# Performance work log

Hardware: AMD Instinct MI355X
Metric: run time of the kernel (lower is better)

## Reference

```python
import jax, jax.numpy as jnp
import numpy as np

TOKENS, DIM, N_EXPERTS, TOPK = 8192, 4096, 256, 8

def setup_inputs() -> dict:
    key = jax.random.key(0)
    k1, k2 = jax.random.split(key)
    x = jax.random.normal(k1, (TOKENS, DIM), dtype=jnp.float32)
    weight = jax.random.normal(k2, (N_EXPERTS, DIM), dtype=jnp.float32) * (DIM ** -0.5)
    return {"x": x, "weight": weight}

def reference(x, weight):
    # logits: [tokens, n_experts]
    logits = jnp.einsum('td,ed->te', x, weight)
    scores = jax.nn.sigmoid(logits)
    topv, indices = jax.lax.top_k(scores, TOPK)          # [tokens, topk]
    gates = topv / jnp.sum(topv, axis=-1, keepdims=True)
    return gates, indices
```

## Files before the change

kernel.cpp:

```cpp
#include <hip/hip_runtime.h>
#include <hip/hip_bf16.h>
#include <hip/hip_fp16.h>
#include <math.h>

#define TOKENS   8192
#define DIM      4096
#define NEXP     256
#define TOPK     8
#define CAND     12

#define MT4      128
#define BK3      64
#define KG       (DIM / 32)

typedef _Float16 f16x8 __attribute__((ext_vector_type(8)));
typedef float    f32x4 __attribute__((ext_vector_type(4)));

typedef const __attribute__((address_space(1))) unsigned int* gas_ptr;
typedef       __attribute__((address_space(3))) unsigned int* las_ptr;

__global__ __launch_bounds__(256)
void convert_w(const float* __restrict__ w, _Float16* __restrict__ whs) {
    const int g = blockIdx.x * 256 + threadIdx.x;
    const int tile = g >> 6, c = g & 63;
    const int q = c >> 4, r = c & 15;
    const int ng = tile / KG, kg = tile % KG;
    const int n = ng * 16 + r, k = kg * 32 + q * 8;
    const float4 a = *(const float4*)(w + (size_t)n * DIM + k);
    const float4 b = *(const float4*)(w + (size_t)n * DIM + k + 4);
    f16x8 h;
    h[0] = (_Float16)a.x; h[1] = (_Float16)a.y;
    h[2] = (_Float16)a.z; h[3] = (_Float16)a.w;
    h[4] = (_Float16)b.x; h[5] = (_Float16)b.y;
    h[6] = (_Float16)b.z; h[7] = (_Float16)b.w;
    *(f16x8*)(whs + (size_t)g * 8) = h;
}

__global__ __launch_bounds__(512, 1)
void gemm_v4(const float* __restrict__ x, const _Float16* __restrict__ whs,
             float* __restrict__ logits, int kspan) {
    __shared__ _Float16 As[2][16 * 512];
    __shared__ _Float16 Bs[2][32 * 512];

    const int t = threadIdx.x, w = t >> 6, lane = t & 63;
    const int wm = w >> 2, wn = w & 3;
    const int m0 = blockIdx.x * MT4;
    const int kb = blockIdx.y * kspan;
    const int kend = kb + kspan;
    float* lp    = logits + (size_t)blockIdx.y * TOKENS * NEXP;

    const int am  = t >> 2;
    const int ack = (t & 3) * 2;
    const int amg = am >> 4, amr = am & 15;
    const int aoff0 = ((amg * 2 + (ack >> 2)) * 64 + (ack & 3) * 16 + amr) * 8;
    const int ack1  = ack + 1;
    const int aoff1 = ((amg * 2 + (ack1 >> 2)) * 64 + (ack1 & 3) * 16 + amr) * 8;

    f32x4 acc[4][4];
    #pragma unroll
    for (int i = 0; i < 4; ++i)
        #pragma unroll
        for (int j = 0; j < 4; ++j) acc[i][j] = (f32x4){0.f, 0.f, 0.f, 0.f};

    const float* xrow = x + (size_t)(m0 + am) * DIM + ack * 8;

    auto stage_B = [&](int buf, int k0) {
        #pragma unroll
        for (int c = 0; c < 4; ++c) {
            const int ti  = w * 4 + c;
            const int ng  = ti >> 1, kgl = ti & 1;
            const _Float16* gp = whs + ((size_t)(ng * KG + (k0 >> 5) + kgl)) * 512
                                     + lane * 8;
            __builtin_amdgcn_global_load_lds((gas_ptr)gp,
                                             (las_ptr)&Bs[buf][ti * 512],
                                             16, 0, 0);
        }
    };
    auto write_A = [&](int buf, const float4& r0, const float4& r1,
                       const float4& r2, const float4& r3) {
        f16x8 h0, h1;
        h0[0] = (_Float16)r0.x; h0[1] = (_Float16)r0.y;
        h0[2] = (_Float16)r0.z; h0[3] = (_Float16)r0.w;
        h0[4] = (_Float16)r1.x; h0[5] = (_Float16)r1.y;
        h0[6] = (_Float16)r1.z; h0[7] = (_Float16)r1.w;
        h1[0] = (_Float16)r2.x; h1[1] = (_Float16)r2.y;
        h1[2] = (_Float16)r2.z; h1[3] = (_Float16)r2.w;
        h1[4] = (_Float16)r3.x; h1[5] = (_Float16)r3.y;
        h1[6] = (_Float16)r3.z; h1[7] = (_Float16)r3.w;
        *(f16x8*)&As[buf][aoff0] = h0;
        *(f16x8*)&As[buf][aoff1] = h1;
    };

    {
        float4 r0 = *(const float4*)(xrow + kb);
        float4 r1 = *(const float4*)(xrow + kb + 4);
        float4 r2 = *(const float4*)(xrow + kb + 8);
        float4 r3 = *(const float4*)(xrow + kb + 12);
        stage_B(0, kb);
        write_A(0, r0, r1, r2, r3);
    }
    float4 xn0, xn1, xn2, xn3;
    if (kb + BK3 < kend) {
        xn0 = *(const float4*)(xrow + kb + BK3);
        xn1 = *(const float4*)(xrow + kb + BK3 + 4);
        xn2 = *(const float4*)(xrow + kb + BK3 + 8);
        xn3 = *(const float4*)(xrow + kb + BK3 + 12);
    }
    __syncthreads();

    int cur = 0;
    for (int k0 = kb; k0 < kend; k0 += BK3) {
        const int nxt = cur ^ 1;
        const bool has_next = (k0 + BK3 < kend);

        if (has_next) stage_B(nxt, k0 + BK3);

        #pragma unroll
        for (int kk = 0; kk < 2; ++kk) {
            f16x8 af[4], bf[4];
            #pragma unroll
            for (int mt = 0; mt < 4; ++mt)
                af[mt] = *(const f16x8*)&As[cur][(((wm * 4 + mt) * 2 + kk) * 64 + lane) * 8];
            #pragma unroll
            for (int nt = 0; nt < 4; ++nt)
                bf[nt] = *(const f16x8*)&Bs[cur][(((wn * 4 + nt) * 2 + kk) * 64 + lane) * 8];
            #pragma unroll
            for (int mt = 0; mt < 4; ++mt)
                #pragma unroll
                for (int nt = 0; nt < 4; ++nt)
                    acc[mt][nt] = __builtin_amdgcn_mfma_f32_16x16x32_f16(
                        af[mt], bf[nt], acc[mt][nt], 0, 0, 0);
        }

        if (has_next) write_A(nxt, xn0, xn1, xn2, xn3);

        __syncthreads();

        if (k0 + 2 * BK3 < kend) {
            xn0 = *(const float4*)(xrow + k0 + 2 * BK3);
            xn1 = *(const float4*)(xrow + k0 + 2 * BK3 + 4);
            xn2 = *(const float4*)(xrow + k0 + 2 * BK3 + 8);
            xn3 = *(const float4*)(xrow + k0 + 2 * BK3 + 12);
        }
        cur = nxt;
    }

    #pragma unroll
    for (int mt = 0; mt < 4; ++mt) {
        #pragma unroll
        for (int nt = 0; nt < 4; ++nt) {
            #pragma unroll
            for (int r = 0; r < 4; ++r) {
                const int m = m0 + (wm * 4 + mt) * 16 + (lane >> 4) * 4 + r;
                const int n = (wn * 4 + nt) * 16 + (lane & 15);
                lp[(size_t)m * NEXP + n] = acc[mt][nt][r];
            }
        }
    }
}

__global__ __launch_bounds__(256)
void topk_cand(const float* __restrict__ logits, int* __restrict__ cand,
               int nsplit) {
    const int lane  = threadIdx.x & 63;
    const int token = blockIdx.x * 4 + (threadIdx.x >> 6);
    const float* lp = logits + (size_t)token * NEXP;

    float s[4];
    #pragma unroll
    for (int j = 0; j < 4; ++j) s[j] = 0.f;
    for (int p = 0; p < nsplit; ++p) {
        const float* pp = lp + (size_t)p * TOKENS * NEXP;
        #pragma unroll
        for (int j = 0; j < 4; ++j) s[j] += pp[j * 64 + lane];
    }

    int mye = 0;
    #pragma unroll
    for (int r = 0; r < CAND; ++r) {
        float bv = s[0];
        int   be = lane;
        #pragma unroll
        for (int j = 1; j < 4; ++j) {
            if (s[j] > bv) { bv = s[j]; be = j * 64 + lane; }
        }
        #pragma unroll
        for (int off = 32; off > 0; off >>= 1) {
            const float ov = __shfl_xor(bv, off, 64);
            const int   oe = __shfl_xor(be, off, 64);
            if (ov > bv || (ov == bv && oe < be)) { bv = ov; be = oe; }
        }
        if (lane == r) mye = be;
        if ((be & 63) == lane) s[be >> 6] = -1e30f;
    }

    if (lane < CAND) cand[token * CAND + lane] = mye;
}

__global__ __launch_bounds__(256)
void rescore(const float* __restrict__ x, const float* __restrict__ w,
             const int* __restrict__ cand, float* __restrict__ out) {
    __shared__ float  xs[DIM];
    __shared__ double stot[CAND];
    __shared__ int    sce[CAND];

    const int t = threadIdx.x, wave = t >> 6, lane = t & 63;
    const int token = blockIdx.x;

    const float* xrow = x + (size_t)token * DIM;
    #pragma unroll
    for (int r = 0; r < 4; ++r) {
        const float* gp = xrow + r * 1024 + wave * 256 + lane * 4;
        __builtin_amdgcn_global_load_lds((gas_ptr)gp,
                                         (las_ptr)&xs[r * 1024 + wave * 256],
                                         16, 0, 2 );
    }

    int ce[3];
    const f32x4* wp[3];
    #pragma unroll
    for (int j = 0; j < 3; ++j) {
        ce[j] = __builtin_amdgcn_readfirstlane(cand[token * CAND + wave * 3 + j]);
        wp[j] = (const f32x4*)(w + (size_t)ce[j] * DIM);
    }

    double acc[3];
    #pragma unroll
    for (int j = 0; j < 3; ++j) acc[j] = 0.0;

    f32x4 wb[4][3];
    #pragma unroll
    for (int j = 0; j < 3; ++j) wb[0][j] = wp[j][lane];
    #pragma unroll
    for (int j = 0; j < 3; ++j) wb[1][j] = wp[j][64 + lane];
    #pragma unroll
    for (int j = 0; j < 3; ++j) wb[2][j] = wp[j][128 + lane];

    __syncthreads();

    #pragma unroll
    for (int i = 0; i < 16; ++i) {
        const int cur = i & 3, nxt = (i + 3) & 3;
        if (i < 13) {
            const int o = lane + (i + 3) * 64;
            #pragma unroll
            for (int j = 0; j < 3; ++j) wb[nxt][j] = wp[j][o];
        }
        const f32x4 xv = *(const f32x4*)&xs[(lane + i * 64) * 4];
        const double dx = (double)xv.x, dy = (double)xv.y;
        const double dz = (double)xv.z, dw = (double)xv.w;
        #pragma unroll
        for (int j = 0; j < 3; ++j) {
            const f32x4 wv = wb[cur][j];
            acc[j] = fma(dw, (double)wv.w,
                     fma(dz, (double)wv.z,
                     fma(dy, (double)wv.y,
                     fma(dx, (double)wv.x, acc[j]))));
        }
    }

    #pragma unroll
    for (int off = 32; off > 0; off >>= 1) {
        #pragma unroll
        for (int j = 0; j < 3; ++j)
            acc[j] += __shfl_xor(acc[j], off, 64);
    }

    if (lane == 0) {
        #pragma unroll
        for (int j = 0; j < 3; ++j) {
            stot[wave * 3 + j] = acc[j];
            sce[wave * 3 + j]  = ce[j];
        }
    }
    __syncthreads();

    if (wave == 0) {
        double tt[CAND];
        int    ee[CAND];
        #pragma unroll
        for (int c = 0; c < CAND; ++c) { tt[c] = stot[c]; ee[c] = sce[c]; }

        int rank[CAND];
        #pragma unroll
        for (int c = 0; c < CAND; ++c) {
            int r = 0;
            #pragma unroll
            for (int j = 0; j < CAND; ++j) {
                if (j == c) continue;
                if (tt[j] > tt[c] || (tt[j] == tt[c] && ee[j] < ee[c])) ++r;
            }
            rank[c] = r;
        }

        float sig[CAND];
        float sum = 0.f;
        #pragma unroll
        for (int c = 0; c < CAND; ++c) {
            sig[c] = 1.0f / (1.0f + expf(-(float)tt[c]));
            if (rank[c] < TOPK) sum += sig[c];
        }

        if (lane < TOPK) {
            float g = 0.f; int ei = 0;
            #pragma unroll
            for (int c = 0; c < CAND; ++c)
                if (rank[c] == lane) { g = sig[c]; ei = ee[c]; }
            out[(size_t)token * TOPK + lane] = g / sum;
            out[(size_t)TOKENS * TOPK + (size_t)token * TOPK + lane] = (float)ei;
        }
    }
}

extern "C" void kernel_launch(void* const* d_in, const int* in_sizes, int n_in,
                              void* d_out, int out_size, void* d_ws, size_t ws_size,
                              hipStream_t stream) {
    const float* x = (const float*)d_in[0];
    const float* w = (const float*)d_in[1];
    float* out     = (float*)d_out;

    const size_t plane = (size_t)TOKENS * NEXP * sizeof(float);
    const size_t fixed = (size_t)TOKENS * CAND * sizeof(int)
                       + (size_t)NEXP * DIM * sizeof(_Float16);
    int S = 4;
    if (ws_size < 4 * plane + fixed) S = (ws_size >= 2 * plane + fixed) ? 2 : 1;

    float*     logits = (float*)d_ws;
    int*       candp  = (int*)((char*)d_ws + (size_t)S * plane);
    _Float16*  whs    = (_Float16*)((char*)candp + (size_t)TOKENS * CAND * sizeof(int));

    convert_w<<<512, 256, 0, stream>>>(w, whs);
    dim3 ggrid(TOKENS / MT4, S);
    gemm_v4<<<ggrid, 512, 0, stream>>>(x, whs, logits, DIM / S);
    topk_cand<<<TOKENS / 4, 256, 0, stream>>>(logits, candp, S);
    rescore<<<TOKENS, 256, 0, stream>>>(x, w, candp, out);
}
```

Before: 311.8 us.

## Triple-buffer GEMM LDS stages with explicit vmcnt waits and raw barriers

```diff
diff --git a/kernel.cpp b/kernel.cpp
--- a/kernel.cpp
+++ b/kernel.cpp
@@ -39,15 +39,15 @@
 __global__ __launch_bounds__(512, 1)
 void gemm_v4(const float* __restrict__ x, const _Float16* __restrict__ whs,
              float* __restrict__ logits, int kspan) {
-    __shared__ _Float16 As[2][16 * 512];
-    __shared__ _Float16 Bs[2][32 * 512];
+    __shared__ _Float16 As[3][16 * 512];
+    __shared__ _Float16 Bs[3][32 * 512];
 
     const int t = threadIdx.x, w = t >> 6, lane = t & 63;
     const int wm = w >> 2, wn = w & 3;
     const int m0 = blockIdx.x * MT4;
     const int kb = blockIdx.y * kspan;
-    const int kend = kb + kspan;
-    float* lp    = logits + (size_t)blockIdx.y * TOKENS * NEXP;
+    const int steps = kspan / BK3;
+    float* lp = logits + (size_t)blockIdx.y * TOKENS * NEXP;
 
     const int am  = t >> 2;
     const int ack = (t & 3) * 2;
@@ -90,40 +90,16 @@
         *(f16x8*)&As[buf][aoff0] = h0;
         *(f16x8*)&As[buf][aoff1] = h1;
     };
-
-    {
-        float4 r0 = *(const float4*)(xrow + kb);
-        float4 r1 = *(const float4*)(xrow + kb + 4);
-        float4 r2 = *(const float4*)(xrow + kb + 8);
-        float4 r3 = *(const float4*)(xrow + kb + 12);
-        stage_B(0, kb);
-        write_A(0, r0, r1, r2, r3);
-    }
-    float4 xn0, xn1, xn2, xn3;
-    if (kb + BK3 < kend) {
-        xn0 = *(const float4*)(xrow + kb + BK3);
-        xn1 = *(const float4*)(xrow + kb + BK3 + 4);
-        xn2 = *(const float4*)(xrow + kb + BK3 + 8);
-        xn3 = *(const float4*)(xrow + kb + BK3 + 12);
-    }
-    __syncthreads();
-
-    int cur = 0;
-    for (int k0 = kb; k0 < kend; k0 += BK3) {
-        const int nxt = cur ^ 1;
-        const bool has_next = (k0 + BK3 < kend);
-
-        if (has_next) stage_B(nxt, k0 + BK3);
-
+    auto compute = [&](int buf) {
         #pragma unroll
         for (int kk = 0; kk < 2; ++kk) {
             f16x8 af[4], bf[4];
             #pragma unroll
             for (int mt = 0; mt < 4; ++mt)
-                af[mt] = *(const f16x8*)&As[cur][(((wm * 4 + mt) * 2 + kk) * 64 + lane) * 8];
+                af[mt] = *(const f16x8*)&As[buf][(((wm * 4 + mt) * 2 + kk) * 64 + lane) * 8];
             #pragma unroll
             for (int nt = 0; nt < 4; ++nt)
-                bf[nt] = *(const f16x8*)&Bs[cur][(((wn * 4 + nt) * 2 + kk) * 64 + lane) * 8];
+                bf[nt] = *(const f16x8*)&Bs[buf][(((wn * 4 + nt) * 2 + kk) * 64 + lane) * 8];
             #pragma unroll
             for (int mt = 0; mt < 4; ++mt)
                 #pragma unroll
@@ -131,18 +107,62 @@
                     acc[mt][nt] = __builtin_amdgcn_mfma_f32_16x16x32_f16(
                         af[mt], bf[nt], acc[mt][nt], 0, 0, 0);
         }
-
-        if (has_next) write_A(nxt, xn0, xn1, xn2, xn3);
-
-        __syncthreads();
-
-        if (k0 + 2 * BK3 < kend) {
-            xn0 = *(const float4*)(xrow + k0 + 2 * BK3);
-            xn1 = *(const float4*)(xrow + k0 + 2 * BK3 + 4);
-            xn2 = *(const float4*)(xrow + k0 + 2 * BK3 + 8);
-            xn3 = *(const float4*)(xrow + k0 + 2 * BK3 + 12);
-        }
-        cur = nxt;
+    };
+    auto wait_vm = [](int k) {
+        switch (k) {
+            case 0:  asm volatile("s_waitcnt vmcnt(0) lgkmcnt(0)"  ::: "memory"); break;
+            case 4:  asm volatile("s_waitcnt vmcnt(4) lgkmcnt(0)"  ::: "memory"); break;
+            case 8:  asm volatile("s_waitcnt vmcnt(8) lgkmcnt(0)"  ::: "memory"); break;
+            case 12: asm volatile("s_waitcnt vmcnt(12) lgkmcnt(0)" ::: "memory"); break;
+            default: asm volatile("s_waitcnt vmcnt(16) lgkmcnt(0)" ::: "memory"); break;
+        }
+    };
+
+    {
+        const float* p0 = xrow + kb;
+        const float* p1 = xrow + kb + BK3;
+        float4 a0 = *(const float4*)(p0),     a1 = *(const float4*)(p0 + 4);
+        float4 a2 = *(const float4*)(p0 + 8), a3 = *(const float4*)(p0 + 12);
+        float4 b0 = *(const float4*)(p1),     b1 = *(const float4*)(p1 + 4);
+        float4 b2 = *(const float4*)(p1 + 8), b3 = *(const float4*)(p1 + 12);
+        stage_B(0, kb);
+        stage_B(1, kb + BK3);
+        write_A(0, a0, a1, a2, a3);
+        write_A(1, b0, b1, b2, b3);
+    }
+    float4 xc0, xc1, xc2, xc3;
+    {
+        const float* p2 = xrow + kb + 2 * BK3;
+        xc0 = *(const float4*)(p2);      xc1 = *(const float4*)(p2 + 4);
+        xc2 = *(const float4*)(p2 + 8);  xc3 = *(const float4*)(p2 + 12);
+    }
+    asm volatile("s_waitcnt vmcnt(0) lgkmcnt(0)" ::: "memory");
+    __builtin_amdgcn_sched_barrier(0);
+    __builtin_amdgcn_s_barrier();
+
+    for (int i = 0; i < steps; ++i) {
+        const int cb = i % 3, sb = (i + 2) % 3;
+        const bool doStage = (i + 2) < steps;
+        const bool doLoadX = (i + 3) < steps;
+
+        if (doStage) write_A(sb, xc0, xc1, xc2, xc3);
+        if (doLoadX) {
+            const float* xp = xrow + kb + (i + 3) * BK3;
+            xc0 = *(const float4*)(xp);      xc1 = *(const float4*)(xp + 4);
+            xc2 = *(const float4*)(xp + 8);  xc3 = *(const float4*)(xp + 12);
+        }
+        if (doStage) stage_B(sb, kb + (i + 2) * BK3);
+
+        const int isP = (i >= 1)
+            ? (((i + 1) < steps ? 4 : 0) + ((i + 2) < steps ? 4 : 0)) : 0;
+        const int isC = ((i + 2) < steps ? 4 : 0) + ((i + 3) < steps ? 4 : 0);
+        wait_vm(isP + isC);
+        __builtin_amdgcn_sched_barrier(0);
+        __builtin_amdgcn_s_barrier();
+
+        compute(cb);
+
+        __builtin_amdgcn_s_barrier();
     }
 
     #pragma unroll
```

New measurement: 306.9 us. No clear change (-1.6%).
